# Kernel optimization log

Measured on AMD Instinct MI355X. Metric: run time of the kernel, lower is better.

## Reference

```python
import jax, jax.numpy as jnp
import numpy as np
import math

N_EMB = 768
N_HEAD = 12
N_INNER = 3072
B, T = 2, 2048
EPS = 1e-4


def _gelu_tanh(x):
    return x * 0.5 * (1.0 + jnp.tanh(math.sqrt(2.0 / math.pi) * (x + 0.044715 * x ** 3)))


def _layernorm(x, scale, bias):
    mean = jnp.mean(x, axis=-1, keepdims=True)
    var = jnp.var(x, axis=-1, keepdims=True, ddof=1)  # torch.var default: unbiased
    return scale * ((x - mean) / jnp.sqrt(var + EPS)) + bias


def setup_inputs() -> dict:
    key = jax.random.key(0)
    ks = jax.random.split(key, 16)
    s_attn = 1.0 / math.sqrt(N_EMB)
    s_mlp1 = 1.0 / math.sqrt(N_EMB)
    s_mlp2 = 1.0 / math.sqrt(N_INNER)
    return {
        "x": jax.random.normal(ks[0], (B, T, N_EMB), dtype=jnp.float32),
        "Wq": jax.random.normal(ks[1], (N_EMB, N_EMB), dtype=jnp.float32) * s_attn,
        "bq": jnp.zeros((N_EMB,), jnp.float32),
        "Wk": jax.random.normal(ks[2], (N_EMB, N_EMB), dtype=jnp.float32) * s_attn,
        "bk": jnp.zeros((N_EMB,), jnp.float32),
        "Wv": jax.random.normal(ks[3], (N_EMB, N_EMB), dtype=jnp.float32) * s_attn,
        "bv": jnp.zeros((N_EMB,), jnp.float32),
        "Wo": jax.random.normal(ks[4], (N_EMB, N_EMB), dtype=jnp.float32) * s_attn,
        "bo": jnp.zeros((N_EMB,), jnp.float32),
        "ln1_s": jnp.ones((N_EMB,), jnp.float32),
        "ln1_b": jnp.zeros((N_EMB,), jnp.float32),
        "W1": jax.random.normal(ks[5], (N_EMB, N_INNER), dtype=jnp.float32) * s_mlp1,
        "b1": jnp.zeros((N_INNER,), jnp.float32),
        "W2": jax.random.normal(ks[6], (N_INNER, N_EMB), dtype=jnp.float32) * s_mlp2,
        "b2": jnp.zeros((N_EMB,), jnp.float32),
        "ln2_s": jnp.ones((N_EMB,), jnp.float32),
        "ln2_b": jnp.zeros((N_EMB,), jnp.float32),
    }


def reference(x, Wq, bq, Wk, bk, Wv, bv, Wo, bo, ln1_s, ln1_b, W1, b1, W2, b2, ln2_s, ln2_b):
    Bx, Tx, C = x.shape
    dh = C // N_HEAD
    # QKV projections -> [B, H, T, dh]
    def split_heads(y):
        return y.reshape(Bx, Tx, N_HEAD, dh).transpose(0, 2, 1, 3)
    q = split_heads(x @ Wq + bq)
    k = split_heads(x @ Wk + bk)
    v = split_heads(x @ Wv + bv)
    # naive full-score causal attention (materializes [B,H,T,T])
    scores = jnp.einsum("bhqd,bhkd->bhqk", q, k)
    causal = jnp.tril(jnp.ones((Tx, Tx), dtype=bool))
    scores = jnp.where(causal, scores, -jnp.inf)
    attn = jax.nn.softmax(scores / math.sqrt(dh), axis=-1)
    ctx = jnp.einsum("bhqk,bhkd->bhqd", attn, v)
    ctx = ctx.transpose(0, 2, 1, 3).reshape(Bx, Tx, C)
    attn_out = ctx @ Wo + bo
    # post-norm residual
    h = _layernorm(x + attn_out, ln1_s, ln1_b)
    mlp_out = _gelu_tanh(h @ W1 + b1) @ W2 + b2
    return _layernorm(h + mlp_out, ln2_s, ln2_b)
```

## Files before the change

### kernel.cpp

```cpp
#include <hip/hip_runtime.h>
#include <math.h>

#define TB  2
#define TT  2048
#define TC  768
#define TH  12
#define TDH 64
#define TI  3072
#define TM  (TB*TT)

typedef __attribute__((ext_vector_type(8))) __bf16 bf16x8;
typedef __attribute__((ext_vector_type(4))) __bf16 bf16x4;
typedef __attribute__((ext_vector_type(4))) float  f32x4;

__device__ __forceinline__ float gelu_tanh(float x) {
    float x3 = x * x * x;
    return 0.5f * x * (1.0f + tanhf(0.7978845608028654f * (x + 0.044715f * x3)));
}

__device__ __forceinline__ void gld_lds16(const void* g, void* l) {
    __builtin_amdgcn_global_load_lds(
        (const __attribute__((address_space(1))) unsigned int*)g,
        (__attribute__((address_space(3))) unsigned int*)l,
        16, 0, 0);
}

#define BK 32

template<int BM_, int BN_, int WM_, int WN_>
__global__ __launch_bounds__(256)
void gemm_mfma(const __bf16* __restrict__ A, const __bf16* __restrict__ Bt,
               const float* __restrict__ b0, const float* __restrict__ b1,
               const float* __restrict__ b2, const float* __restrict__ resid,
               float* __restrict__ outf, __bf16* __restrict__ outb,
               int N, int K, int Kstride, size_t wt_stride, size_t out_stride,
               int ep)
{
    constexpr int WAVES_N = BN_ / WN_;
    constexpr int TMt = WM_ / 16, TNt = WN_ / 16;
    constexpr int AISS = BM_ / 64, BISS = BN_ / 64;
    constexpr int TILE = (BM_ + BN_) * BK;
    __shared__ __align__(16) __bf16 lds[2 * TILE];

    const int tid  = threadIdx.x;
    const int wave = tid >> 6, lane = tid & 63;
    const int wm = wave / WAVES_N, wn = wave % WAVES_N;
    const int m0 = blockIdx.y * BM_, n0 = blockIdx.x * BN_;
    const int z  = blockIdx.z;

    const __bf16* Bz = Bt + (size_t)z * wt_stride;
    const size_t Ksb = (size_t)Kstride * 2;
    const size_t kbaseB = (ep == 3) ? (size_t)z * K * 2 : 0;
    const char* Ag = (const char*)A + (size_t)m0 * Ksb + kbaseB;
    const char* Bg = (const char*)Bz + (size_t)n0 * Ksb + kbaseB;
    const int srow = tid >> 2;
    const int scol = ((tid & 3) ^ ((tid >> 4) & 3)) * 16;
    const int wbase = wave * 1024;

    f32x4 acc[TMt][TNt];
    #pragma unroll
    for (int i = 0; i < TMt; ++i)
        #pragma unroll
        for (int j = 0; j < TNt; ++j)
            acc[i][j] = (f32x4){0.f, 0.f, 0.f, 0.f};

    const int arow = wm * WM_ + (lane & 15);
    const int brow = wn * WN_ + (lane & 15);
    const int koff = (((lane >> 4) ^ ((lane >> 2) & 3))) * 8;

    const int nIter = K / BK;

    auto stage = [&](int buf, int k0b) {
        char* base = (char*)lds + (size_t)buf * TILE * 2;
        #pragma unroll
        for (int s = 0; s < AISS; ++s)
            gld_lds16(Ag + (size_t)(srow + 64 * s) * Ksb + k0b + scol,
                      base + s * 4096 + wbase);
        char* bbase = base + BM_ * BK * 2;
        #pragma unroll
        for (int s = 0; s < BISS; ++s)
            gld_lds16(Bg + (size_t)(srow + 64 * s) * Ksb + k0b + scol,
                      bbase + s * 4096 + wbase);
    };

    stage(0, 0);
    int buf = 0;
    for (int it = 0; it < nIter; ++it) {
        __syncthreads();
        if (it + 1 < nIter) stage(buf ^ 1, (it + 1) * (BK * 2));

        const __bf16* As = lds + (size_t)buf * TILE;
        const __bf16* Bs = As + BM_ * BK;
        bf16x8 af[TMt], bfr[TNt];
        #pragma unroll
        for (int ti = 0; ti < TMt; ++ti)
            af[ti] = *(const bf16x8*)&As[(arow + ti * 16) * BK + koff];
        #pragma unroll
        for (int tj = 0; tj < TNt; ++tj)
            bfr[tj] = *(const bf16x8*)&Bs[(brow + tj * 16) * BK + koff];
        #pragma unroll
        for (int ti = 0; ti < TMt; ++ti)
            #pragma unroll
            for (int tj = 0; tj < TNt; ++tj)
                acc[ti][tj] = __builtin_amdgcn_mfma_f32_16x16x32_bf16(
                    af[ti], bfr[tj], acc[ti][tj], 0, 0, 0);
        buf ^= 1;
    }

    const int lrow = m0 + wm * WM_ + ((lane >> 4) << 2);
    const int lcol = n0 + wn * WN_ + (lane & 15);

    if (ep == 0) {
        const float* bias = (z == 0) ? b0 : (z == 1) ? b1 : b2;
        __bf16* outz = outb + (size_t)z * out_stride;
        if (z < 2) {
            #pragma unroll
            for (int tj = 0; tj < TNt; ++tj) {
                int n = lcol + tj * 16;
                float bj = bias[n];
                int h = n >> 6, d = n & 63;
                #pragma unroll
                for (int ti = 0; ti < TMt; ++ti)
                    #pragma unroll
                    for (int r = 0; r < 4; ++r) {
                        int m = lrow + ti * 16 + r;
                        int b = m >> 11, t = m & (TT - 1);
                        outz[((size_t)(b * TH + h) * TT + t) * TDH + d] =
                            (__bf16)(acc[ti][tj][r] + bj);
                    }
            }
        } else {
            #pragma unroll
            for (int tj = 0; tj < TNt; ++tj) {
                int n = lcol + tj * 16;
                float bj = bias[n];
                int h = n >> 6, d = n & 63;
                #pragma unroll
                for (int ti = 0; ti < TMt; ++ti) {
                    int m = lrow + ti * 16;
                    int b = m >> 11, t0 = m & (TT - 1);
                    bf16x4 pk;
                    #pragma unroll
                    for (int r = 0; r < 4; ++r)
                        pk[r] = (__bf16)(acc[ti][tj][r] + bj);
                    *(bf16x4*)(outz + ((size_t)(b * TH + h) * TDH + d) * TT + t0) = pk;
                }
            }
        }
    } else if (ep == 1) {
        #pragma unroll
        for (int tj = 0; tj < TNt; ++tj) {
            int n = lcol + tj * 16;
            float bj = b0[n];
            #pragma unroll
            for (int ti = 0; ti < TMt; ++ti)
                #pragma unroll
                for (int r = 0; r < 4; ++r) {
                    int m = lrow + ti * 16 + r;
                    outf[(size_t)m * N + n] =
                        acc[ti][tj][r] + bj + resid[(size_t)m * N + n];
                }
        }
    } else if (ep == 2) {
        #pragma unroll
        for (int tj = 0; tj < TNt; ++tj) {
            int n = lcol + tj * 16;
            float bj = b0[n];
            #pragma unroll
            for (int ti = 0; ti < TMt; ++ti)
                #pragma unroll
                for (int r = 0; r < 4; ++r) {
                    int m = lrow + ti * 16 + r;
                    outb[(size_t)m * N + n] = (__bf16)gelu_tanh(acc[ti][tj][r] + bj);
                }
        }
    } else {
        float* outz = outf + (size_t)z * out_stride;
        #pragma unroll
        for (int tj = 0; tj < TNt; ++tj) {
            int n = lcol + tj * 16;
            #pragma unroll
            for (int ti = 0; ti < TMt; ++ti)
                #pragma unroll
                for (int r = 0; r < 4; ++r) {
                    int m = lrow + ti * 16 + r;
                    outz[(size_t)m * N + n] = acc[ti][tj][r];
                }
        }
    }
}

__global__ __launch_bounds__(256)
void prep_kernel(const float* __restrict__ x,
                 const float* __restrict__ Wq, const float* __restrict__ Wk,
                 const float* __restrict__ Wv, const float* __restrict__ Wo,
                 const float* __restrict__ W1, const float* __restrict__ W2,
                 __bf16* __restrict__ x_bf, __bf16* __restrict__ WqkvT,
                 __bf16* __restrict__ WoT, __bf16* __restrict__ W1T,
                 __bf16* __restrict__ W2T)
{
    const size_t WSZ = (size_t)TC * TC;
    int bid = blockIdx.x;
    if (bid < 1536) {
        int i = (bid * 256 + threadIdx.x) * 8;
        float4 a = *(const float4*)(x + i);
        float4 b = *(const float4*)(x + i + 4);
        bf16x8 v;
        v[0] = (__bf16)a.x; v[1] = (__bf16)a.y; v[2] = (__bf16)a.z; v[3] = (__bf16)a.w;
        v[4] = (__bf16)b.x; v[5] = (__bf16)b.y; v[6] = (__bf16)b.z; v[7] = (__bf16)b.w;
        *(bf16x8*)(x_bf + i) = v;
        return;
    }
    bid -= 1536;
    const float* src; __bf16* dst; int K, N, tloc;
    if (bid < 2304) {
        int w = bid / 576; tloc = bid - w * 576;
        K = TC; N = TC;
        src = (w == 0) ? Wq : (w == 1) ? Wk : (w == 2) ? Wv : Wo;
        dst = (w < 3) ? (WqkvT + (size_t)w * WSZ) : WoT;
    } else if (bid < 4608) {
        tloc = bid - 2304; K = TC; N = TI; src = W1; dst = W1T;
    } else {
        tloc = bid - 4608; K = TI; N = TC; src = W2; dst = W2T;
    }
    int tiles_x = N >> 5;
    int n0 = (tloc % tiles_x) * 32, k0 = (tloc / tiles_x) * 32;

    __shared__ float tile[32][33];
    const int tx = threadIdx.x & 31, ty = threadIdx.x >> 5;
    #pragma unroll
    for (int i = 0; i < 32; i += 8)
        tile[ty + i][tx] = src[(size_t)(k0 + ty + i) * N + n0 + tx];
    __syncthreads();
    #pragma unroll
    for (int i = 0; i < 32; i += 8)
        dst[(size_t)(n0 + ty + i) * K + k0 + tx] = (__bf16)tile[tx][ty + i];
}

__device__ __forceinline__ void ln_core(float x0, float x1, float x2,
                                        const float* gs, const float* gb,
                                        float* out_row, __bf16* outbf_row, int tid)
{
    float s = x0 + x1 + x2;
    float q = x0 * x0 + x1 * x1 + x2 * x2;
    #pragma unroll
    for (int off = 32; off > 0; off >>= 1) {
        s += __shfl_down(s, off);
        q += __shfl_down(q, off);
    }
    __shared__ float partial[8];
    __shared__ float stats[2];
    int wid = tid >> 6, lane = tid & 63;
    if (lane == 0) { partial[wid] = s; partial[wid + 4] = q; }
    __syncthreads();
    if (tid == 0) {
        float S = partial[0] + partial[1] + partial[2] + partial[3];
        float Q = partial[4] + partial[5] + partial[6] + partial[7];
        float mean = S * (1.0f / (float)TC);
        float var = (Q - (float)TC * mean * mean) * (1.0f / (float)(TC - 1));
        stats[0] = mean;
        stats[1] = rsqrtf(var + 1e-4f);
    }
    __syncthreads();
    float mean = stats[0], rstd = stats[1];
    float y0 = gs[tid]       * ((x0 - mean) * rstd) + gb[tid];
    float y1 = gs[tid + 256] * ((x1 - mean) * rstd) + gb[tid + 256];
    float y2 = gs[tid + 512] * ((x2 - mean) * rstd) + gb[tid + 512];
    out_row[tid] = y0; out_row[tid + 256] = y1; out_row[tid + 512] = y2;
    if (outbf_row) {
        outbf_row[tid] = (__bf16)y0;
        outbf_row[tid + 256] = (__bf16)y1;
        outbf_row[tid + 512] = (__bf16)y2;
    }
}

__global__ __launch_bounds__(256)
void ln_kernel(const float* __restrict__ in, const float* __restrict__ gs,
               const float* __restrict__ gb, float* __restrict__ out,
               __bf16* __restrict__ out_bf)
{
    const int row = blockIdx.x, tid = threadIdx.x;
    const float* r = in + (size_t)row * TC;
    ln_core(r[tid], r[tid + 256], r[tid + 512], gs, gb,
            out + (size_t)row * TC,
            out_bf ? out_bf + (size_t)row * TC : nullptr, tid);
}

__global__ __launch_bounds__(256)
void ln_fuse(const float* __restrict__ p0, const float* __restrict__ p1,
             const float* __restrict__ bias, const float* __restrict__ resid,
             const float* __restrict__ gs, const float* __restrict__ gb,
             float* __restrict__ out, __bf16* __restrict__ out_bf)
{
    const int row = blockIdx.x, tid = threadIdx.x;
    const size_t o = (size_t)row * TC;
    float x0 = p0[o + tid]       + p1[o + tid]       + bias[tid]       + resid[o + tid];
    float x1 = p0[o + tid + 256] + p1[o + tid + 256] + bias[tid + 256] + resid[o + tid + 256];
    float x2 = p0[o + tid + 512] + p1[o + tid + 512] + bias[tid + 512] + resid[o + tid + 512];
    ln_core(x0, x1, x2, gs, gb, out + o, out_bf ? out_bf + o : nullptr, tid);
}

#define AP 72

__global__ __launch_bounds__(256)
void attn_mfma(const __bf16* __restrict__ Q, const __bf16* __restrict__ K,
               const __bf16* __restrict__ Vt, __bf16* __restrict__ ctx)
{
    __shared__ __align__(16) __bf16 Ks[2][64 * AP];
    __shared__ __align__(16) __bf16 Vs[2][64 * AP];
    __shared__ __align__(16) __bf16 Ps[64 * AP];

    const int tid  = threadIdx.x;
    const int wave = tid >> 6, lane = tid & 63;
    const int c = lane & 15, g = lane >> 4;
    const int bh = blockIdx.y;
    const int qi = blockIdx.x;
    const int qt = (qi & 1) ? (31 - (qi >> 1)) : (qi >> 1);
    const int q_glob = qt * 64 + wave * 16 + c;

    const __bf16* Qb = Q  + (size_t)bh * TT * TDH;
    const __bf16* Kb = K  + (size_t)bh * TT * TDH;
    const __bf16* Vb = Vt + (size_t)bh * TDH * TT;

    bf16x8 qf0 = *(const bf16x8*)(Qb + (size_t)q_glob * TDH + g * 8);
    bf16x8 qf1 = *(const bf16x8*)(Qb + (size_t)q_glob * TDH + 32 + g * 8);

    const int sr = tid >> 3;
    const int sc = (tid & 7) * 8;

    bf16x8 k0 = *(const bf16x8*)(Kb + (size_t)sr * TDH + sc);
    bf16x8 k1 = *(const bf16x8*)(Kb + (size_t)(sr + 32) * TDH + sc);
    bf16x8 v0 = *(const bf16x8*)(Vb + (size_t)sr * TT + sc);
    bf16x8 v1 = *(const bf16x8*)(Vb + (size_t)(sr + 32) * TT + sc);

    float m_i = -1e30f, l_i = 0.0f;
    f32x4 acc[4];
    #pragma unroll
    for (int m2 = 0; m2 < 4; ++m2) acc[m2] = (f32x4){0.f, 0.f, 0.f, 0.f};

    for (int kt = 0; kt <= qt; ++kt) {
        const int b = kt & 1;
        *(bf16x8*)&Ks[b][sr * AP + sc]        = k0;
        *(bf16x8*)&Ks[b][(sr + 32) * AP + sc] = k1;
        *(bf16x8*)&Vs[b][sr * AP + sc]        = v0;
        *(bf16x8*)&Vs[b][(sr + 32) * AP + sc] = v1;
        if (kt < qt) {
            const int o = (kt + 1) * 64;
            k0 = *(const bf16x8*)(Kb + (size_t)(o + sr) * TDH + sc);
            k1 = *(const bf16x8*)(Kb + (size_t)(o + sr + 32) * TDH + sc);
            v0 = *(const bf16x8*)(Vb + (size_t)sr * TT + o + sc);
            v1 = *(const bf16x8*)(Vb + (size_t)(sr + 32) * TT + o + sc);
        }
        __syncthreads();

        f32x4 st[4];
        #pragma unroll
        for (int g2 = 0; g2 < 4; ++g2) {
            bf16x8 af0 = *(const bf16x8*)&Ks[b][(16 * g2 + c) * AP + g * 8];
            bf16x8 af1 = *(const bf16x8*)&Ks[b][(16 * g2 + c) * AP + 32 + g * 8];
            f32x4 z = (f32x4){0.f, 0.f, 0.f, 0.f};
            z = __builtin_amdgcn_mfma_f32_16x16x32_bf16(af0, qf0, z, 0, 0, 0);
            z = __builtin_amdgcn_mfma_f32_16x16x32_bf16(af1, qf1, z, 0, 0, 0);
            st[g2] = z;
        }

        float mx = -1e30f;
        if (kt == qt) {
            #pragma unroll
            for (int g2 = 0; g2 < 4; ++g2)
                #pragma unroll
                for (int r = 0; r < 4; ++r) {
                    int kcol = kt * 64 + 16 * g2 + 4 * g + r;
                    float v = (kcol > q_glob) ? -1e30f : st[g2][r] * 0.125f;
                    st[g2][r] = v;
                    mx = fmaxf(mx, v);
                }
        } else {
            #pragma unroll
            for (int g2 = 0; g2 < 4; ++g2)
                #pragma unroll
                for (int r = 0; r < 4; ++r) {
                    float v = st[g2][r] * 0.125f;
                    st[g2][r] = v;
                    mx = fmaxf(mx, v);
                }
        }
        mx = fmaxf(mx, __shfl_xor(mx, 16));
        mx = fmaxf(mx, __shfl_xor(mx, 32));
        float nm = fmaxf(m_i, mx);
        float corr = __expf(m_i - nm);
        float ps = 0.f;
        #pragma unroll
        for (int g2 = 0; g2 < 4; ++g2) {
            bf16x4 pk;
            #pragma unroll
            for (int r = 0; r < 4; ++r) {
                float p = __expf(st[g2][r] - nm);
                ps += p;
                pk[r] = (__bf16)p;
            }
            *(bf16x4*)&Ps[(wave * 16 + c) * AP + 16 * g2 + 4 * g] = pk;
        }
        ps += __shfl_xor(ps, 16);
        ps += __shfl_xor(ps, 32);
        l_i = l_i * corr + ps;
        m_i = nm;
        #pragma unroll
        for (int m2 = 0; m2 < 4; ++m2) {
            acc[m2][0] *= corr; acc[m2][1] *= corr;
            acc[m2][2] *= corr; acc[m2][3] *= corr;
        }

        bf16x8 pf0 = *(const bf16x8*)&Ps[(wave * 16 + c) * AP + g * 8];
        bf16x8 pf1 = *(const bf16x8*)&Ps[(wave * 16 + c) * AP + 32 + g * 8];
        #pragma unroll
        for (int m2 = 0; m2 < 4; ++m2) {
            bf16x8 vf0 = *(const bf16x8*)&Vs[b][(16 * m2 + c) * AP + g * 8];
            bf16x8 vf1 = *(const bf16x8*)&Vs[b][(16 * m2 + c) * AP + 32 + g * 8];
            acc[m2] = __builtin_amdgcn_mfma_f32_16x16x32_bf16(vf0, pf0, acc[m2], 0, 0, 0);
            acc[m2] = __builtin_amdgcn_mfma_f32_16x16x32_bf16(vf1, pf1, acc[m2], 0, 0, 0);
        }
    }

    const int b = bh / TH, h = bh - b * TH;
    float inv = 1.0f / l_i;
    #pragma unroll
    for (int m2 = 0; m2 < 4; ++m2) {
        bf16x4 o;
        #pragma unroll
        for (int r = 0; r < 4; ++r)
            o[r] = (__bf16)(acc[m2][r] * inv);
        *(bf16x4*)(ctx + ((size_t)b * TT + q_glob) * TC + h * TDH + 16 * m2 + 4 * g) = o;
    }
}

extern "C" void kernel_launch(void* const* d_in, const int* in_sizes, int n_in,
                              void* d_out, int out_size, void* d_ws, size_t ws_size,
                              hipStream_t stream)
{
    const float* x    = (const float*)d_in[0];
    const float* Wq   = (const float*)d_in[1];
    const float* bq   = (const float*)d_in[2];
    const float* Wk   = (const float*)d_in[3];
    const float* bk   = (const float*)d_in[4];
    const float* Wv   = (const float*)d_in[5];
    const float* bv   = (const float*)d_in[6];
    const float* Wo   = (const float*)d_in[7];
    const float* bo   = (const float*)d_in[8];
    const float* ln1s = (const float*)d_in[9];
    const float* ln1b = (const float*)d_in[10];
    const float* W1   = (const float*)d_in[11];
    const float* b1   = (const float*)d_in[12];
    const float* W2   = (const float*)d_in[13];
    const float* b2   = (const float*)d_in[14];
    const float* ln2s = (const float*)d_in[15];
    const float* ln2b = (const float*)d_in[16];
    float* out = (float*)d_out;

    const size_t MC  = (size_t)TM * TC;
    const size_t MCB = MC * 2;
    const size_t WSZ = (size_t)TC * TC;
    const size_t W12 = (size_t)TC * TI;

    char* W = (char*)d_ws;
    __bf16* qkvb  = (__bf16*)W;
    __bf16* x_bf  = (__bf16*)(W + 3 * MCB);
    float*  part0 = (float*)W;
    __bf16* u_bf  = (__bf16*)W;
    float*  h_f32 = (float*)(W + 4 * MCB);
    __bf16* ctxh  = (__bf16*)(W + 6 * MCB);
    __bf16* wts   = (__bf16*)(W + 7 * MCB);
    __bf16* WqkvT = wts;
    __bf16* WoT   = WqkvT + 3 * WSZ;
    __bf16* W1T   = WoT + WSZ;
    __bf16* W2T   = W1T + W12;

    dim3 blk(256);

    prep_kernel<<<dim3(1536 + 6912), blk, 0, stream>>>(
        x, Wq, Wk, Wv, Wo, W1, W2, x_bf, WqkvT, WoT, W1T, W2T);

    gemm_mfma<128, 128, 64, 64><<<dim3(TC / 128, TM / 128, 3), blk, 0, stream>>>(
        x_bf, WqkvT, bq, bk, bv, nullptr, nullptr, qkvb, TC, TC, TC, WSZ, MC, 0);

    attn_mfma<<<dim3(TT / 64, TB * TH), blk, 0, stream>>>(
        qkvb, qkvb + MC, qkvb + 2 * MC, ctxh);

    gemm_mfma<64, 128, 32, 64><<<dim3(TC / 128, TM / 64, 2), blk, 0, stream>>>(
        ctxh, WoT, nullptr, nullptr, nullptr, nullptr, part0, nullptr,
        TC, TC / 2, TC, 0, MC, 3);

    ln_fuse<<<dim3(TM), blk, 0, stream>>>(
        part0, part0 + MC, bo, x, ln1s, ln1b, h_f32, ctxh);

    gemm_mfma<128, 128, 64, 64><<<dim3(TI / 128, TM / 128, 1), blk, 0, stream>>>(
        ctxh, W1T, b1, nullptr, nullptr, nullptr, nullptr, u_bf, TI, TC, TC, 0, 0, 2);

    gemm_mfma<64, 128, 32, 64><<<dim3(TC / 128, TM / 64, 1), blk, 0, stream>>>(
        u_bf, W2T, b2, nullptr, nullptr, h_f32, out, nullptr, TC, TI, TI, 0, 0, 1);

    ln_kernel<<<dim3(TM), blk, 0, stream>>>(out, ln2s, ln2b, out, nullptr);
}
```

Before: 324.6 us.

## Split-K GEMMs across more blocks and fuse final residual into layernorm

Adds a bf16 split-K epilogue (ep 4) and switches the W2 GEMM to a two-way split-K whose bf16 partials are summed with bias and residual inside a new fused layernorm kernel. The separate residual-epilogue GEMM plus standalone layernorm are replaced. The Wo GEMM becomes a three-way split-K with a three-input fused layernorm, and the QKV and W1 GEMMs move to smaller 64x128 tiles to launch more blocks. This trades extra partial-sum traffic for better CU occupancy. Storing W2 partials in bf16 adds rounding error to the pre-norm sum.

```diff
diff --git a/kernel.cpp b/kernel.cpp
--- a/kernel.cpp
+++ b/kernel.cpp
@@ -50,7 +50,7 @@
 
     const __bf16* Bz = Bt + (size_t)z * wt_stride;
     const size_t Ksb = (size_t)Kstride * 2;
-    const size_t kbaseB = (ep == 3) ? (size_t)z * K * 2 : 0;
+    const size_t kbaseB = (ep >= 3) ? (size_t)z * K * 2 : 0;
     const char* Ag = (const char*)A + (size_t)m0 * Ksb + kbaseB;
     const char* Bg = (const char*)Bz + (size_t)n0 * Ksb + kbaseB;
     const int srow = tid >> 2;
@@ -174,7 +174,7 @@
                     outb[(size_t)m * N + n] = (__bf16)gelu_tanh(acc[ti][tj][r] + bj);
                 }
         }
-    } else {
+    } else if (ep == 3) {
         float* outz = outf + (size_t)z * out_stride;
         #pragma unroll
         for (int tj = 0; tj < TNt; ++tj) {
@@ -185,6 +185,19 @@
                 for (int r = 0; r < 4; ++r) {
                     int m = lrow + ti * 16 + r;
                     outz[(size_t)m * N + n] = acc[ti][tj][r];
+                }
+        }
+    } else {
+        __bf16* outz = outb + (size_t)z * out_stride;
+        #pragma unroll
+        for (int tj = 0; tj < TNt; ++tj) {
+            int n = lcol + tj * 16;
+            #pragma unroll
+            for (int ti = 0; ti < TMt; ++ti)
+                #pragma unroll
+                for (int r = 0; r < 4; ++r) {
+                    int m = lrow + ti * 16 + r;
+                    outz[(size_t)m * N + n] = (__bf16)acc[ti][tj][r];
                 }
         }
     }
@@ -275,29 +288,32 @@
 }
 
 __global__ __launch_bounds__(256)
-void ln_kernel(const float* __restrict__ in, const float* __restrict__ gs,
-               const float* __restrict__ gb, float* __restrict__ out,
-               __bf16* __restrict__ out_bf)
-{
-    const int row = blockIdx.x, tid = threadIdx.x;
-    const float* r = in + (size_t)row * TC;
-    ln_core(r[tid], r[tid + 256], r[tid + 512], gs, gb,
-            out + (size_t)row * TC,
-            out_bf ? out_bf + (size_t)row * TC : nullptr, tid);
-}
-
-__global__ __launch_bounds__(256)
-void ln_fuse(const float* __restrict__ p0, const float* __restrict__ p1,
-             const float* __restrict__ bias, const float* __restrict__ resid,
-             const float* __restrict__ gs, const float* __restrict__ gb,
-             float* __restrict__ out, __bf16* __restrict__ out_bf)
+void ln_fuse3(const float* __restrict__ p0, const float* __restrict__ p1,
+              const float* __restrict__ p2, const float* __restrict__ bias,
+              const float* __restrict__ resid,
+              const float* __restrict__ gs, const float* __restrict__ gb,
+              float* __restrict__ out, __bf16* __restrict__ out_bf)
 {
     const int row = blockIdx.x, tid = threadIdx.x;
     const size_t o = (size_t)row * TC;
-    float x0 = p0[o + tid]       + p1[o + tid]       + bias[tid]       + resid[o + tid];
-    float x1 = p0[o + tid + 256] + p1[o + tid + 256] + bias[tid + 256] + resid[o + tid + 256];
-    float x2 = p0[o + tid + 512] + p1[o + tid + 512] + bias[tid + 512] + resid[o + tid + 512];
+    float x0 = p0[o + tid]       + p1[o + tid]       + p2[o + tid]       + bias[tid]       + resid[o + tid];
+    float x1 = p0[o + tid + 256] + p1[o + tid + 256] + p2[o + tid + 256] + bias[tid + 256] + resid[o + tid + 256];
+    float x2 = p0[o + tid + 512] + p1[o + tid + 512] + p2[o + tid + 512] + bias[tid + 512] + resid[o + tid + 512];
     ln_core(x0, x1, x2, gs, gb, out + o, out_bf ? out_bf + o : nullptr, tid);
+}
+
+__global__ __launch_bounds__(256)
+void ln_fuse2b(const __bf16* __restrict__ p0, const __bf16* __restrict__ p1,
+               const float* __restrict__ bias, const float* __restrict__ resid,
+               const float* __restrict__ gs, const float* __restrict__ gb,
+               float* __restrict__ out)
+{
+    const int row = blockIdx.x, tid = threadIdx.x;
+    const size_t o = (size_t)row * TC;
+    float x0 = (float)p0[o + tid]       + (float)p1[o + tid]       + bias[tid]       + resid[o + tid];
+    float x1 = (float)p0[o + tid + 256] + (float)p1[o + tid + 256] + bias[tid + 256] + resid[o + tid + 256];
+    float x2 = (float)p0[o + tid + 512] + (float)p1[o + tid + 512] + bias[tid + 512] + resid[o + tid + 512];
+    ln_core(x0, x1, x2, gs, gb, out + o, nullptr, tid);
 }
 
 #define AP 72
@@ -466,9 +482,11 @@
     __bf16* qkvb  = (__bf16*)W;
     __bf16* x_bf  = (__bf16*)(W + 3 * MCB);
     float*  part0 = (float*)W;
+    float*  part2 = (float*)(W + 4 * MCB);
     __bf16* u_bf  = (__bf16*)W;
     float*  h_f32 = (float*)(W + 4 * MCB);
     __bf16* ctxh  = (__bf16*)(W + 6 * MCB);
+    __bf16* p0b   = (__bf16*)(W + 6 * MCB);
     __bf16* wts   = (__bf16*)(W + 7 * MCB);
     __bf16* WqkvT = wts;
     __bf16* WoT   = WqkvT + 3 * WSZ;
@@ -480,24 +498,26 @@
     prep_kernel<<<dim3(1536 + 6912), blk, 0, stream>>>(
         x, Wq, Wk, Wv, Wo, W1, W2, x_bf, WqkvT, WoT, W1T, W2T);
 
-    gemm_mfma<128, 128, 64, 64><<<dim3(TC / 128, TM / 128, 3), blk, 0, stream>>>(
+    gemm_mfma<64, 128, 32, 64><<<dim3(TC / 128, TM / 64, 3), blk, 0, stream>>>(
         x_bf, WqkvT, bq, bk, bv, nullptr, nullptr, qkvb, TC, TC, TC, WSZ, MC, 0);
 
     attn_mfma<<<dim3(TT / 64, TB * TH), blk, 0, stream>>>(
         qkvb, qkvb + MC, qkvb + 2 * MC, ctxh);
 
+    gemm_mfma<64, 128, 32, 64><<<dim3(TC / 128, TM / 64, 3), blk, 0, stream>>>(
+        ctxh, WoT, nullptr, nullptr, nullptr, nullptr, part0, nullptr,
+        TC, TC / 3, TC, 0, MC, 3);
+
+    ln_fuse3<<<dim3(TM), blk, 0, stream>>>(
+        part0, part0 + MC, part2, bo, x, ln1s, ln1b, h_f32, ctxh);
+
+    gemm_mfma<64, 128, 32, 64><<<dim3(TI / 128, TM / 64, 1), blk, 0, stream>>>(
+        ctxh, W1T, b1, nullptr, nullptr, nullptr, nullptr, u_bf, TI, TC, TC, 0, 0, 2);
+
     gemm_mfma<64, 128, 32, 64><<<dim3(TC / 128, TM / 64, 2), blk, 0, stream>>>(
-        ctxh, WoT, nullptr, nullptr, nullptr, nullptr, part0, nullptr,
-        TC, TC / 2, TC, 0, MC, 3);
-
-    ln_fuse<<<dim3(TM), blk, 0, stream>>>(
-        part0, part0 + MC, bo, x, ln1s, ln1b, h_f32, ctxh);
-
-    gemm_mfma<128, 128, 64, 64><<<dim3(TI / 128, TM / 128, 1), blk, 0, stream>>>(
-        ctxh, W1T, b1, nullptr, nullptr, nullptr, nullptr, u_bf, TI, TC, TC, 0, 0, 2);
-
-    gemm_mfma<64, 128, 32, 64><<<dim3(TC / 128, TM / 64, 1), blk, 0, stream>>>(
-        u_bf, W2T, b2, nullptr, nullptr, h_f32, out, nullptr, TC, TI, TI, 0, 0, 1);
-
-    ln_kernel<<<dim3(TM), blk, 0, stream>>>(out, ln2s, ln2b, out, nullptr);
-}
+        u_bf, W2T, nullptr, nullptr, nullptr, nullptr, nullptr, p0b,
+        TC, TI / 2, TI, 0, MC, 4);
+
+    ln_fuse2b<<<dim3(TM), blk, 0, stream>>>(
+        p0b, p0b + MC, b2, h_f32, ln2s, ln2b, out);
+}
```

New measurement: 325.0 us. Within noise of the previous version (+0.1%).
